# Performance work log

Hardware: AMD Instinct MI355X
Metric: run time of the kernel (lower is better)

Reference implementation:

```python
import jax, jax.numpy as jnp
import numpy as np

B = 2097152
T = 4      # num_tokens
E = 16     # attn_embed_dim
H = 32     # hidden_dim
O = 16     # output_dim


def _xavier(key, shape):
    fan_out, fan_in = shape
    std = np.sqrt(2.0 / (fan_in + fan_out)).astype(np.float32)
    return jax.random.normal(key, shape, dtype=jnp.float32) * std


def setup_inputs() -> dict:
    key = jax.random.key(0)
    ks = jax.random.split(key, 7)
    x = jax.random.normal(ks[0], (B, 1), dtype=jnp.float32)
    # initial_fc: Linear(1 -> T*E)
    W0 = _xavier(ks[1], (T * E, 1)); b0 = jnp.zeros((T * E,), jnp.float32)
    # MultiheadAttention packed in-projection: [3E, E]
    Wqkv = _xavier(ks[2], (3 * E, E)); bqkv = jnp.zeros((3 * E,), jnp.float32)
    # out_proj: Linear(E -> E)
    Wo = _xavier(ks[3], (E, E)); bo = jnp.zeros((E,), jnp.float32)
    # post_fc: Linear(E -> H), LeakyReLU(0.01), Linear(H -> O)
    W1 = _xavier(ks[4], (H, E)); b1 = jnp.zeros((H,), jnp.float32)
    W2 = _xavier(ks[5], (O, H)); b2 = jnp.zeros((O,), jnp.float32)
    return {"x": x, "W0": W0, "b0": b0, "Wqkv": Wqkv, "bqkv": bqkv,
            "Wo": Wo, "bo": bo, "W1": W1, "b1": b1, "W2": W2, "b2": b2}


def reference(x, W0, b0, Wqkv, bqkv, Wo, bo, W1, b1, W2, b2):
    b = x.shape[0]
    scale = jnp.float32(1.0 / np.sqrt(E))
    # expand scalar -> tokens [B, T, E]
    tokens = (x @ W0.T + b0).reshape(b, T, E)
    # packed QKV projection (PyTorch MHA, 1 head)
    qkv = jnp.einsum('bte,fe->btf', tokens, Wqkv) + bqkv  # [B, T, 3E]
    q, k, v = jnp.split(qkv, 3, axis=-1)
    scores = jnp.einsum('bqe,bke->bqk', q, k) * scale     # [B, T, T]
    attn = jax.nn.softmax(scores, axis=-1)
    ctx = jnp.einsum('bqk,bke->bqe', attn, v)             # [B, T, E]
    attn_out = ctx @ Wo.T + bo
    pooled = attn_out.mean(axis=1)                        # [B, E]
    h = jax.nn.leaky_relu(pooled @ W1.T + b1, negative_slope=0.01)
    return h @ W2.T + b2                                  # [B, O]
```

## Files before the change

kernel.cpp:

```cpp
#include <hip/hip_runtime.h>
#include <hip/hip_bf16.h>


#define WS_SA 0
#define WS_SB 16
#define WS_SC 32
#define WS_A1 48
#define WS_A2 1072
#define WS_A3 1584
#define WS_BC 2096
#define WS_K8 2608

using f32x4 = __attribute__((ext_vector_type(4))) float;
using bf16x8 = __attribute__((ext_vector_type(8))) short;

union FragU {
  unsigned u[4];
  bf16x8 v;
};

__device__ inline f32x4 mfma16(bf16x8 a, bf16x8 b, f32x4 c) {
  return __builtin_amdgcn_mfma_f32_16x16x32_bf16(a, b, c, 0, 0, 0);
}

__device__ inline unsigned short bf16_rne(float f) {
  unsigned u = __float_as_uint(f);
  unsigned lsb = (u >> 16) & 1u;
  u += 0x7fffu + lsb;
  return (unsigned short)(u >> 16);
}
__device__ inline float bf16_f32(unsigned short h) {
  return __uint_as_float(((unsigned)h) << 16);
}
__device__ inline unsigned pack2(unsigned short lo, unsigned short hi) {
  return (unsigned)lo | ((unsigned)hi << 16);
}
__device__ inline unsigned cvt2(float a, float b) {
  unsigned r;
  asm("v_cvt_pk_bf16_f32 %0, %1, %2" : "=v"(r) : "v"(a), "v"(b));
  return r;
}
__device__ inline float lo_f32(unsigned u) { return __uint_as_float(u << 16); }
__device__ inline float hi_f32(unsigned u) {
  return __uint_as_float(u & 0xffff0000u);
}
__device__ inline float uni(float v) {
  return __int_as_float(__builtin_amdgcn_readfirstlane(__float_as_int(v)));
}

__global__ __launch_bounds__(256) void precompute_kernel(
    const float* __restrict__ W0, const float* __restrict__ b0,
    const float* __restrict__ Wqkv, const float* __restrict__ bqkv,
    const float* __restrict__ Wo, const float* __restrict__ bo,
    const float* __restrict__ W1, const float* __restrict__ b1,
    const float* __restrict__ W2, const float* __restrict__ b2,
    float* __restrict__ wsf) {
  unsigned* wsu = (unsigned*)wsf;
  __shared__ float P[4][48], Q[4][48], Wc[32][16];
  __shared__ float M[32][8], bcs[32], W2M[16][8], c8[16];
  const int tid = threadIdx.x;

  for (int idx = tid; idx < 4 * 48; idx += 256) {
    int t = idx / 48, f = idx % 48;
    float p = 0.f, q = 0.f;
    for (int e = 0; e < 16; ++e) {
      float w = Wqkv[f * 16 + e];
      p += W0[t * 16 + e] * w;
      q += b0[t * 16 + e] * w;
    }
    P[t][f] = p;
    Q[t][f] = q + bqkv[f];
  }
  for (int idx = tid; idx < 32 * 16; idx += 256) {
    int h = idx / 16, e = idx % 16;
    float acc = 0.f;
    for (int ep = 0; ep < 16; ++ep) acc += W1[h * 16 + ep] * Wo[ep * 16 + e];
    Wc[h][e] = acc;
  }
  __syncthreads();

  const float SCL = 0.25f * 1.4426950408889634f;
  for (int idx = tid; idx < 16; idx += 256) {
    int i = idx / 4, j = idx % 4;
    float a = 0.f, b = 0.f, c = 0.f;
    for (int e = 0; e < 16; ++e) {
      float pq = P[i][e], qq = Q[i][e];
      float pk = P[j][16 + e], qk = Q[j][16 + e];
      a += pq * pk;
      b += pq * qk + qq * pk;
      c += qq * qk;
    }
    wsf[WS_SA + idx] = a * SCL;
    wsf[WS_SB + idx] = b * SCL;
    wsf[WS_SC + idx] = c * SCL;
  }
  for (int idx = tid; idx < 32; idx += 256) {
    float acc = b1[idx];
    for (int ep = 0; ep < 16; ++ep) acc += W1[idx * 16 + ep] * bo[ep];
    bcs[idx] = acc;
  }
  for (int idx = tid; idx < 256; idx += 256) {
    int h = idx >> 3, k = idx & 7, j = k & 3;
    float acc = 0.f;
    if (k < 4)
      for (int e = 0; e < 16; ++e) acc += Wc[h][e] * P[j][32 + e];
    else
      for (int e = 0; e < 16; ++e) acc += Wc[h][e] * Q[j][32 + e];
    M[h][k] = 0.25f * acc;
  }
  __syncthreads();
  for (int idx = tid; idx < 128; idx += 256) {
    int o = idx >> 3, k = idx & 7;
    float acc = 0.f;
    for (int h = 0; h < 32; ++h) acc += W2[o * 32 + h] * M[h][k];
    W2M[o][k] = acc;
  }
  for (int idx = tid; idx < 16; idx += 256) {
    float acc = 0.f;
    for (int h = 0; h < 32; ++h) acc += W2[idx * 32 + h] * bcs[h];
    c8[idx] = acc;
  }
  __syncthreads();

  if (tid < 64) {
    const int lane = tid;
    const int g = lane >> 4, row = lane & 15;
    for (int hb = 0; hb < 2; ++hb) {
      int h = 16 * hb + row;
      for (int dw = 0; dw < 4; ++dw) {
        float m0 = (g == 0) ? M[h][2 * dw] : 0.f;
        float m1 = (g == 0) ? M[h][2 * dw + 1] : 0.f;
        unsigned short h0 = bf16_rne(m0), h1 = bf16_rne(m1);
        unsigned short l0 = bf16_rne(m0 - bf16_f32(h0));
        unsigned short l1 = bf16_rne(m1 - bf16_f32(h1));
        wsu[WS_A1 + ((hb * 2 + 0) * 64 + lane) * 4 + dw] = pack2(h0, h1);
        wsu[WS_A1 + ((hb * 2 + 1) * 64 + lane) * 4 + dw] = pack2(l0, l1);
      }
    }
    for (int dw = 0; dw < 4; ++dw) {
      float m0 = (g == 0) ? 0.505f * W2M[row][2 * dw] : 0.f;
      float m1 = (g == 0) ? 0.505f * W2M[row][2 * dw + 1] : 0.f;
      unsigned short h0 = bf16_rne(m0), h1 = bf16_rne(m1);
      unsigned short l0 = bf16_rne(m0 - bf16_f32(h0));
      unsigned short l1 = bf16_rne(m1 - bf16_f32(h1));
      wsu[WS_A2 + (0 * 64 + lane) * 4 + dw] = pack2(h0, h1);
      wsu[WS_A2 + (1 * 64 + lane) * 4 + dw] = pack2(l0, l1);
    }
    for (int dw = 0; dw < 4; ++dw) {
      int j0 = 2 * dw, j1 = 2 * dw + 1;
      int H0 = (j0 < 4) ? 4 * g + j0 : 16 + 4 * g + (j0 - 4);
      int H1 = (j1 < 4) ? 4 * g + j1 : 16 + 4 * g + (j1 - 4);
      float m0 = 0.495f * W2[row * 32 + H0];
      float m1 = 0.495f * W2[row * 32 + H1];
      unsigned short h0 = bf16_rne(m0), h1 = bf16_rne(m1);
      unsigned short l0 = bf16_rne(m0 - bf16_f32(h0));
      unsigned short l1 = bf16_rne(m1 - bf16_f32(h1));
      wsu[WS_A3 + (0 * 64 + lane) * 4 + dw] = pack2(h0, h1);
      wsu[WS_A3 + (1 * 64 + lane) * 4 + dw] = pack2(l0, l1);
    }
    for (int hb = 0; hb < 2; ++hb)
      for (int r = 0; r < 4; ++r)
        wsf[WS_BC + lane * 8 + hb * 4 + r] = bcs[16 * hb + 4 * g + r];
    for (int r = 0; r < 4; ++r)
      wsf[WS_K8 + lane * 4 + r] = 0.505f * c8[4 * g + r] + b2[4 * g + r];
  }
}

__global__ __launch_bounds__(256) void subnet_mfma_kernel(
    const float* __restrict__ x, const float* __restrict__ wsf,
    float* __restrict__ out, int B) {
  const unsigned* wsu = (const unsigned*)wsf;
  const int lane = threadIdx.x & 63;
  const int wave = blockIdx.x * (blockDim.x >> 6) + (threadIdx.x >> 6);
  const int g = lane >> 4;

  FragU A1h0, A1l0, A1h1, A1l1, A2h, A2l, A3h, A3l;
#pragma unroll
  for (int dw = 0; dw < 4; ++dw) {
    A1h0.u[dw] = wsu[WS_A1 + ((0) * 64 + lane) * 4 + dw];
    A1l0.u[dw] = wsu[WS_A1 + ((1) * 64 + lane) * 4 + dw];
    A1h1.u[dw] = wsu[WS_A1 + ((2) * 64 + lane) * 4 + dw];
    A1l1.u[dw] = wsu[WS_A1 + ((3) * 64 + lane) * 4 + dw];
    A2h.u[dw] = wsu[WS_A2 + (0 * 64 + lane) * 4 + dw];
    A2l.u[dw] = wsu[WS_A2 + (1 * 64 + lane) * 4 + dw];
    A3h.u[dw] = wsu[WS_A3 + (0 * 64 + lane) * 4 + dw];
    A3l.u[dw] = wsu[WS_A3 + (1 * 64 + lane) * 4 + dw];
  }
  f32x4 bc0, bc1, k8;
#pragma unroll
  for (int r = 0; r < 4; ++r) {
    bc0[r] = wsf[WS_BC + lane * 8 + r];
    bc1[r] = wsf[WS_BC + lane * 8 + 4 + r];
    k8[r] = wsf[WS_K8 + lane * 4 + r];
  }
  float sa[16], sb[16], sc[16];
#pragma unroll
  for (int i = 0; i < 16; ++i) {
    sa[i] = uni(wsf[WS_SA + i]);
    sb[i] = uni(wsf[WS_SB + i]);
    sc[i] = uni(wsf[WS_SC + i]);
  }
  const int permidx = (lane & 15) * 4;
  const long nchunk = (long)(B >> 6);

  float xs4[4];
#pragma unroll
  for (int ci = 0; ci < 4; ++ci) {
    const long chunk = (long)wave * 4 + ci;
    xs4[ci] = (chunk < nchunk)
                  ? __builtin_nontemporal_load(x + chunk * 64 + lane)
                  : 0.f;
  }

#pragma unroll 1
  for (int ci = 0; ci < 4; ++ci) {
    const long chunk = (long)wave * 4 + ci;
    if (chunk >= nchunk) break;
    const long ebase = chunk * 64;
    const float xx = xs4[ci];

    float s0 = 0.f, s1 = 0.f, s2 = 0.f, s3 = 0.f;
#pragma unroll
    for (int i = 0; i < 4; ++i) {
      float r0 = (sa[i * 4 + 0] * xx + sb[i * 4 + 0]) * xx + sc[i * 4 + 0];
      float r1 = (sa[i * 4 + 1] * xx + sb[i * 4 + 1]) * xx + sc[i * 4 + 1];
      float r2 = (sa[i * 4 + 2] * xx + sb[i * 4 + 2]) * xx + sc[i * 4 + 2];
      float r3 = (sa[i * 4 + 3] * xx + sb[i * 4 + 3]) * xx + sc[i * 4 + 3];
      float p0 = __builtin_amdgcn_exp2f(r0);
      float p1 = __builtin_amdgcn_exp2f(r1);
      float p2 = __builtin_amdgcn_exp2f(r2);
      float p3 = __builtin_amdgcn_exp2f(r3);
      float rinv = __builtin_amdgcn_rcpf(p0 + p1 + p2 + p3);
      s0 += p0 * rinv;
      s1 += p1 * rinv;
      s2 += p2 * rinv;
      s3 += p3 * rinv;
    }

    float gv[8] = {xx * s0, xx * s1, xx * s2, xx * s3, s0, s1, s2, s3};
    unsigned gh[4], gl[4];
#pragma unroll
    for (int d = 0; d < 4; ++d) {
      unsigned ph = cvt2(gv[2 * d], gv[2 * d + 1]);
      gh[d] = ph;
      gl[d] = cvt2(gv[2 * d] - lo_f32(ph), gv[2 * d + 1] - hi_f32(ph));
    }

#pragma unroll
    for (int eg = 0; eg < 4; ++eg) {
      const int pidx = permidx + 64 * eg;
      FragU Bh, Bl;
#pragma unroll
      for (int d = 0; d < 4; ++d) {
        Bh.u[d] = (unsigned)__builtin_amdgcn_ds_bpermute(pidx, (int)gh[d]);
        Bl.u[d] = (unsigned)__builtin_amdgcn_ds_bpermute(pidx, (int)gl[d]);
      }
      f32x4 z0 = bc0, z1 = bc1;
      z0 = mfma16(A1h0.v, Bh.v, z0);
      z1 = mfma16(A1h1.v, Bh.v, z1);
      z0 = mfma16(A1l0.v, Bh.v, z0);
      z1 = mfma16(A1l1.v, Bh.v, z1);
      z0 = mfma16(A1h0.v, Bl.v, z0);
      z1 = mfma16(A1h1.v, Bl.v, z1);
      float za[8];
      za[0] = fabsf(z0[0]); za[1] = fabsf(z0[1]);
      za[2] = fabsf(z0[2]); za[3] = fabsf(z0[3]);
      za[4] = fabsf(z1[0]); za[5] = fabsf(z1[1]);
      za[6] = fabsf(z1[2]); za[7] = fabsf(z1[3]);
      FragU Zh, Zl;
#pragma unroll
      for (int d = 0; d < 4; ++d) {
        unsigned ph = cvt2(za[2 * d], za[2 * d + 1]);
        Zh.u[d] = ph;
        Zl.u[d] = cvt2(za[2 * d] - lo_f32(ph), za[2 * d + 1] - hi_f32(ph));
      }
      f32x4 acc = k8;
      acc = mfma16(A3h.v, Zh.v, acc);
      acc = mfma16(A3l.v, Zh.v, acc);
      acc = mfma16(A3h.v, Zl.v, acc);
      acc = mfma16(A2h.v, Bh.v, acc);
      acc = mfma16(A2l.v, Bh.v, acc);
      acc = mfma16(A2h.v, Bl.v, acc);
      const long e = ebase + 16 * eg + (lane & 15);
      __builtin_nontemporal_store(
          acc, reinterpret_cast<f32x4*>(out + e * 16 + 4 * g));
    }
  }
}

extern "C" void kernel_launch(void* const* d_in, const int* in_sizes, int n_in,
                              void* d_out, int out_size, void* d_ws,
                              size_t ws_size, hipStream_t stream) {
  const float* x = (const float*)d_in[0];
  const float* W0 = (const float*)d_in[1];
  const float* b0 = (const float*)d_in[2];
  const float* Wqkv = (const float*)d_in[3];
  const float* bqkv = (const float*)d_in[4];
  const float* Wo = (const float*)d_in[5];
  const float* bo = (const float*)d_in[6];
  const float* W1 = (const float*)d_in[7];
  const float* b1 = (const float*)d_in[8];
  const float* W2 = (const float*)d_in[9];
  const float* b2 = (const float*)d_in[10];
  float* out = (float*)d_out;
  float* ws = (float*)d_ws;

  const int B = in_sizes[0];

  precompute_kernel<<<1, 256, 0, stream>>>(W0, b0, Wqkv, bqkv, Wo, bo, W1, b1,
                                           W2, b2, ws);

  const int blocks = (B + 1023) / 1024;
  subnet_mfma_kernel<<<blocks, 256, 0, stream>>>(x, ws, out, B);
}
```

Baseline: 40.64 us.

## Fuse weight precompute into main kernel, recomputing per block into LDS

```diff
diff --git a/kernel.cpp b/kernel.cpp
--- a/kernel.cpp
+++ b/kernel.cpp
@@ -40,6 +40,11 @@
   asm("v_cvt_pk_bf16_f32 %0, %1, %2" : "=v"(r) : "v"(a), "v"(b));
   return r;
 }
+__device__ inline unsigned cvt2abs(float a, float b) {
+  unsigned r;
+  asm("v_cvt_pk_bf16_f32 %0, abs(%1), abs(%2)" : "=v"(r) : "v"(a), "v"(b));
+  return r;
+}
 __device__ inline float lo_f32(unsigned u) { return __uint_as_float(u << 16); }
 __device__ inline float hi_f32(unsigned u) {
   return __uint_as_float(u & 0xffff0000u);
@@ -48,16 +53,16 @@
   return __int_as_float(__builtin_amdgcn_readfirstlane(__float_as_int(v)));
 }
 
-__global__ __launch_bounds__(256) void precompute_kernel(
-    const float* __restrict__ W0, const float* __restrict__ b0,
-    const float* __restrict__ Wqkv, const float* __restrict__ bqkv,
-    const float* __restrict__ Wo, const float* __restrict__ bo,
-    const float* __restrict__ W1, const float* __restrict__ b1,
-    const float* __restrict__ W2, const float* __restrict__ b2,
-    float* __restrict__ wsf) {
-  unsigned* wsu = (unsigned*)wsf;
+__global__ __launch_bounds__(256) void subnet_fused_kernel(
+    const float* __restrict__ x, const float* __restrict__ W0,
+    const float* __restrict__ b0, const float* __restrict__ Wqkv,
+    const float* __restrict__ bqkv, const float* __restrict__ Wo,
+    const float* __restrict__ bo, const float* __restrict__ W1,
+    const float* __restrict__ b1, const float* __restrict__ W2,
+    const float* __restrict__ b2, float* __restrict__ out, int B) {
   __shared__ float P[4][48], Q[4][48], Wc[32][16];
   __shared__ float M[32][8], bcs[32], W2M[16][8], c8[16];
+  __shared__ float LF[2864];
   const int tid = threadIdx.x;
 
   for (int idx = tid; idx < 4 * 48; idx += 256) {
@@ -90,9 +95,9 @@
       b += pq * qk + qq * pk;
       c += qq * qk;
     }
-    wsf[WS_SA + idx] = a * SCL;
-    wsf[WS_SB + idx] = b * SCL;
-    wsf[WS_SC + idx] = c * SCL;
+    LF[WS_SA + idx] = a * SCL;
+    LF[WS_SB + idx] = b * SCL;
+    LF[WS_SC + idx] = c * SCL;
   }
   for (int idx = tid; idx < 32; idx += 256) {
     float acc = b1[idx];
@@ -123,53 +128,51 @@
   __syncthreads();
 
   if (tid < 64) {
+    unsigned* lfu = (unsigned*)LF;
     const int lane = tid;
-    const int g = lane >> 4, row = lane & 15;
+    const int gg = lane >> 4, row = lane & 15;
     for (int hb = 0; hb < 2; ++hb) {
       int h = 16 * hb + row;
       for (int dw = 0; dw < 4; ++dw) {
-        float m0 = (g == 0) ? M[h][2 * dw] : 0.f;
-        float m1 = (g == 0) ? M[h][2 * dw + 1] : 0.f;
+        float m0 = (gg == 0) ? M[h][2 * dw] : 0.f;
+        float m1 = (gg == 0) ? M[h][2 * dw + 1] : 0.f;
         unsigned short h0 = bf16_rne(m0), h1 = bf16_rne(m1);
         unsigned short l0 = bf16_rne(m0 - bf16_f32(h0));
         unsigned short l1 = bf16_rne(m1 - bf16_f32(h1));
-        wsu[WS_A1 + ((hb * 2 + 0) * 64 + lane) * 4 + dw] = pack2(h0, h1);
-        wsu[WS_A1 + ((hb * 2 + 1) * 64 + lane) * 4 + dw] = pack2(l0, l1);
+        lfu[WS_A1 + ((hb * 2 + 0) * 64 + lane) * 4 + dw] = pack2(h0, h1);
+        lfu[WS_A1 + ((hb * 2 + 1) * 64 + lane) * 4 + dw] = pack2(l0, l1);
       }
     }
     for (int dw = 0; dw < 4; ++dw) {
-      float m0 = (g == 0) ? 0.505f * W2M[row][2 * dw] : 0.f;
-      float m1 = (g == 0) ? 0.505f * W2M[row][2 * dw + 1] : 0.f;
+      float m0 = (gg == 0) ? 0.505f * W2M[row][2 * dw] : 0.f;
+      float m1 = (gg == 0) ? 0.505f * W2M[row][2 * dw + 1] : 0.f;
       unsigned short h0 = bf16_rne(m0), h1 = bf16_rne(m1);
       unsigned short l0 = bf16_rne(m0 - bf16_f32(h0));
       unsigned short l1 = bf16_rne(m1 - bf16_f32(h1));
-      wsu[WS_A2 + (0 * 64 + lane) * 4 + dw] = pack2(h0, h1);
-      wsu[WS_A2 + (1 * 64 + lane) * 4 + dw] = pack2(l0, l1);
+      lfu[WS_A2 + (0 * 64 + lane) * 4 + dw] = pack2(h0, h1);
+      lfu[WS_A2 + (1 * 64 + lane) * 4 + dw] = pack2(l0, l1);
     }
     for (int dw = 0; dw < 4; ++dw) {
       int j0 = 2 * dw, j1 = 2 * dw + 1;
-      int H0 = (j0 < 4) ? 4 * g + j0 : 16 + 4 * g + (j0 - 4);
-      int H1 = (j1 < 4) ? 4 * g + j1 : 16 + 4 * g + (j1 - 4);
+      int H0 = (j0 < 4) ? 4 * gg + j0 : 16 + 4 * gg + (j0 - 4);
+      int H1 = (j1 < 4) ? 4 * gg + j1 : 16 + 4 * gg + (j1 - 4);
       float m0 = 0.495f * W2[row * 32 + H0];
       float m1 = 0.495f * W2[row * 32 + H1];
       unsigned short h0 = bf16_rne(m0), h1 = bf16_rne(m1);
       unsigned short l0 = bf16_rne(m0 - bf16_f32(h0));
       unsigned short l1 = bf16_rne(m1 - bf16_f32(h1));
-      wsu[WS_A3 + (0 * 64 + lane) * 4 + dw] = pack2(h0, h1);
-      wsu[WS_A3 + (1 * 64 + lane) * 4 + dw] = pack2(l0, l1);
+      lfu[WS_A3 + (0 * 64 + lane) * 4 + dw] = pack2(h0, h1);
+      lfu[WS_A3 + (1 * 64 + lane) * 4 + dw] = pack2(l0, l1);
     }
     for (int hb = 0; hb < 2; ++hb)
       for (int r = 0; r < 4; ++r)
-        wsf[WS_BC + lane * 8 + hb * 4 + r] = bcs[16 * hb + 4 * g + r];
+        LF[WS_BC + lane * 8 + hb * 4 + r] = bcs[16 * hb + 4 * gg + r];
     for (int r = 0; r < 4; ++r)
-      wsf[WS_K8 + lane * 4 + r] = 0.505f * c8[4 * g + r] + b2[4 * g + r];
-  }
-}
-
-__global__ __launch_bounds__(256) void subnet_mfma_kernel(
-    const float* __restrict__ x, const float* __restrict__ wsf,
-    float* __restrict__ out, int B) {
-  const unsigned* wsu = (const unsigned*)wsf;
+      LF[WS_K8 + lane * 4 + r] = 0.505f * c8[4 * gg + r] + b2[4 * gg + r];
+  }
+  __syncthreads();
+
+  const unsigned* lfu = (const unsigned*)LF;
   const int lane = threadIdx.x & 63;
   const int wave = blockIdx.x * (blockDim.x >> 6) + (threadIdx.x >> 6);
   const int g = lane >> 4;
@@ -177,46 +180,46 @@
   FragU A1h0, A1l0, A1h1, A1l1, A2h, A2l, A3h, A3l;
 #pragma unroll
   for (int dw = 0; dw < 4; ++dw) {
-    A1h0.u[dw] = wsu[WS_A1 + ((0) * 64 + lane) * 4 + dw];
-    A1l0.u[dw] = wsu[WS_A1 + ((1) * 64 + lane) * 4 + dw];
-    A1h1.u[dw] = wsu[WS_A1 + ((2) * 64 + lane) * 4 + dw];
-    A1l1.u[dw] = wsu[WS_A1 + ((3) * 64 + lane) * 4 + dw];
-    A2h.u[dw] = wsu[WS_A2 + (0 * 64 + lane) * 4 + dw];
-    A2l.u[dw] = wsu[WS_A2 + (1 * 64 + lane) * 4 + dw];
-    A3h.u[dw] = wsu[WS_A3 + (0 * 64 + lane) * 4 + dw];
-    A3l.u[dw] = wsu[WS_A3 + (1 * 64 + lane) * 4 + dw];
+    A1h0.u[dw] = lfu[WS_A1 + ((0) * 64 + lane) * 4 + dw];
+    A1l0.u[dw] = lfu[WS_A1 + ((1) * 64 + lane) * 4 + dw];
+    A1h1.u[dw] = lfu[WS_A1 + ((2) * 64 + lane) * 4 + dw];
+    A1l1.u[dw] = lfu[WS_A1 + ((3) * 64 + lane) * 4 + dw];
+    A2h.u[dw] = lfu[WS_A2 + (0 * 64 + lane) * 4 + dw];
+    A2l.u[dw] = lfu[WS_A2 + (1 * 64 + lane) * 4 + dw];
+    A3h.u[dw] = lfu[WS_A3 + (0 * 64 + lane) * 4 + dw];
+    A3l.u[dw] = lfu[WS_A3 + (1 * 64 + lane) * 4 + dw];
   }
   f32x4 bc0, bc1, k8;
 #pragma unroll
   for (int r = 0; r < 4; ++r) {
-    bc0[r] = wsf[WS_BC + lane * 8 + r];
-    bc1[r] = wsf[WS_BC + lane * 8 + 4 + r];
-    k8[r] = wsf[WS_K8 + lane * 4 + r];
+    bc0[r] = LF[WS_BC + lane * 8 + r];
+    bc1[r] = LF[WS_BC + lane * 8 + 4 + r];
+    k8[r] = LF[WS_K8 + lane * 4 + r];
   }
   float sa[16], sb[16], sc[16];
 #pragma unroll
   for (int i = 0; i < 16; ++i) {
-    sa[i] = uni(wsf[WS_SA + i]);
-    sb[i] = uni(wsf[WS_SB + i]);
-    sc[i] = uni(wsf[WS_SC + i]);
+    sa[i] = uni(LF[WS_SA + i]);
+    sb[i] = LF[WS_SB + i];
+    sc[i] = uni(LF[WS_SC + i]);
   }
   const int permidx = (lane & 15) * 4;
   const long nchunk = (long)(B >> 6);
 
+  const float* xp = x + (long)wave * 256 + lane;
   float xs4[4];
 #pragma unroll
   for (int ci = 0; ci < 4; ++ci) {
     const long chunk = (long)wave * 4 + ci;
-    xs4[ci] = (chunk < nchunk)
-                  ? __builtin_nontemporal_load(x + chunk * 64 + lane)
-                  : 0.f;
-  }
+    xs4[ci] = (chunk < nchunk) ? __builtin_nontemporal_load(xp + ci * 64) : 0.f;
+  }
+
+  float* op = out + ((long)wave * 256 + (lane & 15)) * 16 + 4 * g;
 
 #pragma unroll 1
   for (int ci = 0; ci < 4; ++ci) {
     const long chunk = (long)wave * 4 + ci;
     if (chunk >= nchunk) break;
-    const long ebase = chunk * 64;
     const float xx = xs4[ci];
 
     float s0 = 0.f, s1 = 0.f, s2 = 0.f, s3 = 0.f;
@@ -262,17 +265,16 @@
       z1 = mfma16(A1l1.v, Bh.v, z1);
       z0 = mfma16(A1h0.v, Bl.v, z0);
       z1 = mfma16(A1h1.v, Bl.v, z1);
-      float za[8];
-      za[0] = fabsf(z0[0]); za[1] = fabsf(z0[1]);
-      za[2] = fabsf(z0[2]); za[3] = fabsf(z0[3]);
-      za[4] = fabsf(z1[0]); za[5] = fabsf(z1[1]);
-      za[6] = fabsf(z1[2]); za[7] = fabsf(z1[3]);
+      float zz[8];
+      zz[0] = z0[0]; zz[1] = z0[1]; zz[2] = z0[2]; zz[3] = z0[3];
+      zz[4] = z1[0]; zz[5] = z1[1]; zz[6] = z1[2]; zz[7] = z1[3];
       FragU Zh, Zl;
 #pragma unroll
       for (int d = 0; d < 4; ++d) {
-        unsigned ph = cvt2(za[2 * d], za[2 * d + 1]);
+        unsigned ph = cvt2abs(zz[2 * d], zz[2 * d + 1]);
         Zh.u[d] = ph;
-        Zl.u[d] = cvt2(za[2 * d] - lo_f32(ph), za[2 * d + 1] - hi_f32(ph));
+        Zl.u[d] = cvt2(fabsf(zz[2 * d]) - lo_f32(ph),
+                       fabsf(zz[2 * d + 1]) - hi_f32(ph));
       }
       f32x4 acc = k8;
       acc = mfma16(A3h.v, Zh.v, acc);
@@ -281,10 +283,10 @@
       acc = mfma16(A2h.v, Bh.v, acc);
       acc = mfma16(A2l.v, Bh.v, acc);
       acc = mfma16(A2h.v, Bl.v, acc);
-      const long e = ebase + 16 * eg + (lane & 15);
-      __builtin_nontemporal_store(
-          acc, reinterpret_cast<f32x4*>(out + e * 16 + 4 * g));
-    }
+      __builtin_nontemporal_store(acc,
+                                  reinterpret_cast<f32x4*>(op + eg * 256));
+    }
+    op += 1024;
   }
 }
 
@@ -303,13 +305,9 @@
   const float* W2 = (const float*)d_in[9];
   const float* b2 = (const float*)d_in[10];
   float* out = (float*)d_out;
-  float* ws = (float*)d_ws;
 
   const int B = in_sizes[0];
-
-  precompute_kernel<<<1, 256, 0, stream>>>(W0, b0, Wqkv, bqkv, Wo, bo, W1, b1,
-                                           W2, b2, ws);
-
   const int blocks = (B + 1023) / 1024;
-  subnet_mfma_kernel<<<blocks, 256, 0, stream>>>(x, ws, out, B);
-}
+  subnet_fused_kernel<<<blocks, 256, 0, stream>>>(x, W0, b0, Wqkv, bqkv, Wo,
+                                                  bo, W1, b1, W2, b2, out, B);
+}
```

New measurement: 45.02 us. 1.11x slower.
